# Performance work log

Hardware: AMD Instinct MI355X
Metric: run time of the kernel (lower is better)

## Reference

```python
import jax, jax.numpy as jnp
import numpy as np

L_DEG = 4      # max out-degree L
DEPTH = 7      # complete L-ary tree depth -> 21845 nodes
N_GEN = 16
C_ST = 8
M_LAB = 256


def _build_tree():
    sizes = [L_DEG ** d for d in range(DEPTH + 1)]
    limits = np.concatenate([[0], np.cumsum(sizes)]).astype(np.int64)
    t_size = int(limits[-1])
    nodes = np.arange(t_size)
    rng = np.random.default_rng(0)
    labels = rng.integers(0, M_LAB, t_size)
    parent = np.where(nodes > 0, (nodes - 1) // L_DEG, 0)
    pos = np.where(nodes > 0, (nodes - 1) % L_DEG, 0)
    ch = np.zeros((t_size, L_DEG), dtype=np.int64)
    n_internal = int(limits[-2])
    ch[:n_internal] = L_DEG * nodes[:n_internal, None] + np.arange(1, L_DEG + 1)[None, :]
    t = np.concatenate([labels[:, None], parent[:, None], pos[:, None], ch], axis=1).astype(np.int64)
    return t, limits


def setup_inputs() -> dict:
    key = jax.random.key(0)
    ka, kb, kp, ks = jax.random.split(key, 4)
    t, limits = _build_tree()
    return {
        "t": jnp.asarray(t),
        "t_limits": jnp.asarray(limits),
        "a": jax.random.normal(ka, (N_GEN, C_ST, C_ST, L_DEG), dtype=jnp.float32),
        "b": jax.random.normal(kb, (N_GEN, C_ST, M_LAB), dtype=jnp.float32),
        "pi": jax.random.normal(kp, (N_GEN, C_ST, L_DEG), dtype=jnp.float32),
        "sp": jax.random.normal(ks, (N_GEN, L_DEG), dtype=jnp.float32),
    }


def _forward(tn, lim, a, b, pi, sp):
    # tn, lim are host numpy int arrays (tree structure is a constant).
    G, C, _, L = a.shape
    t_size = int(lim[-1])
    n_levels = len(lim) - 1
    sL = int(lim[-2])                      # first leaf index
    labels = tn[:, 0]
    posf = tn[:, 2]
    ch_all = tn[:, 3:3 + L]

    sm_a = jax.nn.softmax(a, axis=1)       # P(parent_state i | child_state j, pos l)
    sm_b = jax.nn.softmax(b, axis=2)
    sm_pi = jax.nn.softmax(pi, axis=1)
    sm_sp = jax.nn.softmax(sp, axis=1)
    a_sp = sm_a * sm_sp[:, None, None, :]  # [G,i,j,L]

    # ---------------- upward pass ----------------
    prior = jnp.zeros((t_size, G, C), a.dtype)
    beta = jnp.zeros((t_size, G, C), a.dtype)
    beta_il = jnp.zeros((t_size, G, C), a.dtype)

    prior_lv = jnp.moveaxis(sm_pi[:, :, posf[sL:]], 2, 0)   # [NL,G,C]
    emis_lv = jnp.moveaxis(sm_b[:, :, labels[sL:]], 2, 0)   # [NL,G,C]
    beta_lv = prior_lv * emis_lv
    beta_lv = beta_lv / jnp.sum(beta_lv, axis=2, keepdims=True)
    prior = prior.at[sL:].set(prior_lv)
    beta = beta.at[sL:].set(beta_lv)

    for lev in range(n_levels - 2, -1, -1):   # internal levels, bottom-up
        s, e = int(lim[lev]), int(lim[lev + 1])
        ch = ch_all[s:e]                       # [P,L]
        mask = (ch > 0).astype(a.dtype)        # children packed in first slots
        prior_ch = prior[ch]                   # [P,L,G,C]
        beta_ch = beta[ch]                     # [P,L,G,C]
        u_prior = jnp.einsum('gijl,pl,plgj->pgi', a_sp, mask, prior_ch)
        u_bil = jnp.einsum('gijl,pl,plgj->pgi', a_sp, mask, beta_ch) / u_prior
        emis = jnp.moveaxis(sm_b[:, :, labels[s:e]], 2, 0)  # [P,G,C]
        tmp = emis * u_bil * u_prior
        u_beta = tmp / jnp.sum(tmp, axis=2, keepdims=True)
        prior = prior.at[s:e].set(u_prior)
        beta = beta.at[s:e].set(u_beta)
        beta_il = beta_il.at[s:e].set(u_bil)

    # ---------------- downward pass ----------------
    # row t_size is a dummy slot for padded (absent) children
    eps_i = jnp.zeros((t_size + 1, G, C), a.dtype).at[0].set(beta[0])
    eps_ijl = jnp.zeros((t_size, G, C, C, L), a.dtype)
    for lev in range(0, n_levels - 1):         # parents, top-down (root included)
        s, e = int(lim[lev]), int(lim[lev + 1])
        ch = ch_all[s:e]
        maskb = ch > 0
        mask = maskb.astype(a.dtype)
        beta_ch = jnp.transpose(beta[ch], (0, 2, 3, 1))       # [P,G,Cj,L]
        pe = eps_i[s:e] / (prior[s:e] * beta_il[s:e])         # [P,G,Ci]
        res = (pe[:, :, :, None, None] * a_sp[None]
               * beta_ch[:, :, None, :, :]
               * mask[:, None, None, None, :])                # [P,G,i,j,L]
        child_eps = jnp.sum(res, axis=3)                       # sum over j (as in source) -> [P,G,i,L]
        vals = jnp.moveaxis(child_eps, 3, 1).reshape(-1, G, C) # [P*L,G,C]
        safe = np.where(maskb, ch, t_size).reshape(-1)
        eps_i = eps_i.at[safe].set(vals)
        eps_ijl = eps_ijl.at[s:e].set(res)
    eps_i = eps_i[:t_size]
    # leaves' eps_ijl stay zero (source scatters zeros there)

    # ---------------- log-likelihood ----------------
    a_lh = jnp.einsum('ugijl,gijl->g', eps_ijl, jnp.log(sm_a))
    b_lh = jnp.einsum('ugc,gcu->g', eps_i, jnp.log(sm_b)[:, :, labels])
    pi_lh = jnp.einsum('ugc,gcu->g', eps_i[sL:], jnp.log(sm_pi)[:, :, posf[sL:]])
    eps_l = jnp.sum(eps_ijl, axis=(2, 3))                      # [u,g,L]
    sp_lh = jnp.einsum('ugl,gl->g', eps_l, jnp.log(sm_sp))
    return a_lh + b_lh + pi_lh + sp_lh


def reference(t, t_limits, a, b, pi, sp):
    tn = np.asarray(t)
    lim = np.asarray(t_limits)
    return _forward(tn, lim, a, b, pi, sp)
```

## Files before the change

### kernel.cpp

```cpp
#include <hip/hip_runtime.h>


#define G 16
#define C 8
#define GC 128
#define TSIZE 21845
#define SL 5461

__device__ __forceinline__ float grp8_sum(float v) {
  v += __shfl_xor(v, 1);
  v += __shfl_xor(v, 2);
  v += __shfl_xor(v, 4);
  return v;
}

__global__ void setup_kernel(const float* __restrict__ ain, const float* __restrict__ bin,
                             const float* __restrict__ piin, const float* __restrict__ spin,
                             float* __restrict__ a_sp, float* __restrict__ log_a,
                             float* __restrict__ sm_bT, float* __restrict__ log_bT,
                             float* __restrict__ sm_piT, float* __restrict__ log_piT,
                             float* __restrict__ log_sp, unsigned* __restrict__ ctr) {
  int blk = blockIdx.x, tid = threadIdx.x;
  if (blk < 16) {
    int g = blk;
    __shared__ float red4[4];
    for (int c = 0; c < 8; ++c) {
      int row = g * 8 + c;
      float x = bin[row * 256 + tid];
      float m = x;
      #pragma unroll
      for (int off2 = 32; off2; off2 >>= 1) m = fmaxf(m, __shfl_xor(m, off2));
      if ((tid & 63) == 0) red4[tid >> 6] = m;
      __syncthreads();
      m = fmaxf(fmaxf(red4[0], red4[1]), fmaxf(red4[2], red4[3]));
      __syncthreads();
      float e = expf(x - m);
      float ssum = e;
      #pragma unroll
      for (int off2 = 32; off2; off2 >>= 1) ssum += __shfl_xor(ssum, off2);
      if ((tid & 63) == 0) red4[tid >> 6] = ssum;
      __syncthreads();
      ssum = red4[0] + red4[1] + red4[2] + red4[3];
      __syncthreads();
      sm_bT[tid * GC + row]  = e / ssum;
      log_bT[tid * GC + row] = (x - m) - logf(ssum);
    }
  } else if (blk == 16) {
    for (int col = tid; col < 512; col += 256) {
      int g = col >> 5, j = (col >> 2) & 7, l = col & 3;
      float x[8], m = -1e30f;
      #pragma unroll
      for (int i = 0; i < 8; ++i) { x[i] = ain[g*256 + i*32 + j*4 + l]; m = fmaxf(m, x[i]); }
      float ssum = 0.f;
      #pragma unroll
      for (int i = 0; i < 8; ++i) ssum += expf(x[i] - m);
      float ls = logf(ssum);
      float y0 = spin[g*4+0], y1 = spin[g*4+1], y2 = spin[g*4+2], y3 = spin[g*4+3];
      float ms = fmaxf(fmaxf(y0, y1), fmaxf(y2, y3));
      float d = expf(y0-ms) + expf(y1-ms) + expf(y2-ms) + expf(y3-ms);
      float spv = expf(spin[g*4+l] - ms) / d;
      #pragma unroll
      for (int i = 0; i < 8; ++i) {
        int o2 = g*256 + i*32 + j*4 + l;
        float smv = expf(x[i] - m) / ssum;
        a_sp[o2]  = smv * spv;
        log_a[o2] = (x[i] - m) - ls;
      }
    }
  } else {
    if (tid < 64) {
      int g = tid >> 2, l = tid & 3;
      float x[8], m = -1e30f;
      #pragma unroll
      for (int c = 0; c < 8; ++c) { x[c] = piin[g*32 + c*4 + l]; m = fmaxf(m, x[c]); }
      float ssum = 0.f;
      #pragma unroll
      for (int c = 0; c < 8; ++c) ssum += expf(x[c] - m);
      float ls = logf(ssum);
      #pragma unroll
      for (int c = 0; c < 8; ++c) {
        sm_piT[l*GC + g*8 + c]  = expf(x[c] - m) / ssum;
        log_piT[l*GC + g*8 + c] = (x[c] - m) - ls;
      }
    } else if (tid < 80) {
      int g = tid - 64;
      float y[4], m = -1e30f;
      #pragma unroll
      for (int l = 0; l < 4; ++l) { y[l] = spin[g*4 + l]; m = fmaxf(m, y[l]); }
      float ssum = 0.f;
      #pragma unroll
      for (int l = 0; l < 4; ++l) ssum += expf(y[l] - m);
      float ls = logf(ssum);
      #pragma unroll
      for (int l = 0; l < 4; ++l) log_sp[g*4 + l] = (y[l] - m) - ls;
    } else if (tid == 80) {
      *ctr = 0u;
    }
  }
}

__device__ __forceinline__ void up_lds(int v, int lab, int gi, int g8,
    const float* asp, const float* __restrict__ sm_bT,
    float* sBeta, float* sNum, bool wantNum) {
  int ch0 = 4*v + 1;
  float ub = 0.f;
  #pragma unroll
  for (int l = 0; l < 4; ++l) {
    const float4* bp = (const float4*)(sBeta + (ch0 + l)*GC + g8);
    float4 b0 = bp[0], b1 = bp[1];
    ub += asp[l]*b0.x + asp[4+l]*b0.y + asp[8+l]*b0.z + asp[12+l]*b0.w
        + asp[16+l]*b1.x + asp[20+l]*b1.y + asp[24+l]*b1.z + asp[28+l]*b1.w;
  }
  float tmp = sm_bT[lab*GC + gi] * ub;
  float s = grp8_sum(tmp);
  sBeta[v*GC + gi] = tmp / s;
  if (wantNum) sNum[v*GC + gi] = ub;
}

__device__ __forceinline__ double down_lds(int v, int lab, float e, int gi, int g8,
    const float* asp, const float* aal, const float* lsp,
    const float* __restrict__ log_bT, float* sBeta, const float* sNum) {
  float pe = e / sNum[v*GC + gi];
  int ch0 = 4*v + 1;
  float local = 0.f;
  #pragma unroll
  for (int l = 0; l < 4; ++l) {
    float4* bp = (float4*)(sBeta + (ch0 + l)*GC + g8);
    float4 b0 = bp[0], b1 = bp[1];
    float S = asp[l]*b0.x + asp[4+l]*b0.y + asp[8+l]*b0.z + asp[12+l]*b0.w
            + asp[16+l]*b1.x + asp[20+l]*b1.y + asp[24+l]*b1.z + asp[28+l]*b1.w;
    float A = aal[l]*b0.x + aal[4+l]*b0.y + aal[8+l]*b0.z + aal[12+l]*b0.w
            + aal[16+l]*b1.x + aal[20+l]*b1.y + aal[24+l]*b1.z + aal[28+l]*b1.w;
    float ce = pe * S;
    sBeta[(ch0 + l)*GC + gi] = ce;
    local += pe*A + ce*lsp[l];
  }
  return (double)local + (double)(e * log_bT[lab*GC + gi]);
}

__global__ __launch_bounds__(512, 1) void up_kernel(
    const float* __restrict__ a_sp, const float* __restrict__ sm_bT,
    const float* __restrict__ sm_piT, const int* __restrict__ t,
    float* __restrict__ betaG) {
  __shared__ float sBeta[85*GC];
  const int blk = blockIdx.x, tid = threadIdx.x;
  const int gi = tid & 127, g = gi >> 3, i = gi & 7, g8 = g*8, w = tid >> 7;
  float asp[32];
  {
    const float4* pa = (const float4*)(a_sp + g*256 + i*32);
    #pragma unroll
    for (int q = 0; q < 8; ++q) {
      float4 v = pa[q];
      asp[q*4+0]=v.x; asp[q*4+1]=v.y; asp[q*4+2]=v.z; asp[q*4+3]=v.w;
    }
  }
  const int base_leaf = SL + blk*64;
  #pragma unroll
  for (int it = 0; it < 16; ++it) {
    int k = it*4 + w;
    float bt = sm_piT[(k & 3)*GC + gi] * sm_bT[t[(base_leaf + k)*7]*GC + gi];
    float s = grp8_sum(bt);
    sBeta[(21 + k)*GC + gi] = bt / s;
  }
  __syncthreads();
  #pragma unroll
  for (int it = 0; it < 4; ++it) {
    int k = it*4 + w;
    up_lds(5 + k, t[(1365 + blk*16 + k)*7], gi, g8, asp, sm_bT, sBeta, nullptr, false);
  }
  __syncthreads();
  up_lds(1 + w, t[(341 + blk*4 + w)*7], gi, g8, asp, sm_bT, sBeta, nullptr, false);
  __syncthreads();
  if (tid < 128) {
    up_lds(0, t[(85 + blk)*7], gi, g8, asp, sm_bT, sBeta, nullptr, false);
    betaG[(size_t)(85 + blk)*GC + gi] = sBeta[gi];
  }
}

__global__ __launch_bounds__(512, 1) void downall_kernel(
    const float* __restrict__ a_sp, const float* __restrict__ log_a,
    const float* __restrict__ log_sp, const float* __restrict__ sm_bT,
    const float* __restrict__ log_bT, const float* __restrict__ sm_piT,
    const float* __restrict__ log_piT, const int* __restrict__ t,
    const float* __restrict__ betaG, unsigned* __restrict__ ctr,
    double* __restrict__ partial, float* __restrict__ out) {
  __shared__ float  sBeta[85*GC];
  __shared__ float  sNum[21*GC];
  __shared__ float  sEps[GC];
  __shared__ double sd[64];
  __shared__ double sfin[256];
  __shared__ unsigned lastFlag;
  const int blk = blockIdx.x, tid = threadIdx.x;
  const int gi = tid & 127, g = gi >> 3, i = gi & 7, g8 = g*8, w = tid >> 7;
  float asp[32], aal[32], lsp[4];
  {
    const float4* pa = (const float4*)(a_sp  + g*256 + i*32);
    const float4* pl = (const float4*)(log_a + g*256 + i*32);
    #pragma unroll
    for (int k = 0; k < 8; ++k) {
      float4 va = pa[k], vl = pl[k];
      asp[k*4+0]=va.x; asp[k*4+1]=va.y; asp[k*4+2]=va.z; asp[k*4+3]=va.w;
      aal[k*4+0]=va.x*vl.x; aal[k*4+1]=va.y*vl.y; aal[k*4+2]=va.z*vl.z; aal[k*4+3]=va.w*vl.w;
    }
    #pragma unroll
    for (int l = 0; l < 4; ++l) lsp[l] = log_sp[g*4 + l];
  }

  #pragma unroll
  for (int it = 0; it < 16; ++it) {
    int k = it*4 + w, u = 21 + k;
    int ch0 = 4*u + 1;
    float ub = 0.f;
    #pragma unroll
    for (int l = 0; l < 4; ++l) {
      const float4* bp = (const float4*)(betaG + (size_t)(ch0 + l)*GC + g8);
      float4 b0 = bp[0], b1 = bp[1];
      ub += asp[l]*b0.x + asp[4+l]*b0.y + asp[8+l]*b0.z + asp[12+l]*b0.w
          + asp[16+l]*b1.x + asp[20+l]*b1.y + asp[24+l]*b1.z + asp[28+l]*b1.w;
    }
    float tmp = sm_bT[t[u*7]*GC + gi] * ub;
    float s = grp8_sum(tmp);
    sBeta[u*GC + gi] = tmp / s;
  }
  __syncthreads();
  #pragma unroll
  for (int it = 0; it < 4; ++it) {
    int u = 5 + it*4 + w;
    up_lds(u, t[u*7], gi, g8, asp, sm_bT, sBeta, sNum, true);
  }
  __syncthreads();
  up_lds(1 + w, t[(1 + w)*7], gi, g8, asp, sm_bT, sBeta, sNum, true);
  __syncthreads();
  if (tid < 128)
    up_lds(0, t[0], gi, g8, asp, sm_bT, sBeta, sNum, true);
  __syncthreads();

  double acc = 0.0;
  if (tid < 128) {
    int a1 = 1 + (blk >> 6), a2 = 5 + (blk >> 4), a3 = 21 + (blk >> 2);
    float e = sBeta[gi];
    int anc[3] = {0, a1, a2};
    int chn[3] = {a1, a2, a3};
    #pragma unroll
    for (int s2 = 0; s2 < 3; ++s2) {
      float pe = e / sNum[anc[s2]*GC + gi];
      int l = (chn[s2] - 1) & 3;
      const float4* bp = (const float4*)(sBeta + chn[s2]*GC + g8);
      float4 b0 = bp[0], b1 = bp[1];
      float S = asp[l]*b0.x + asp[4+l]*b0.y + asp[8+l]*b0.z + asp[12+l]*b0.w
              + asp[16+l]*b1.x + asp[20+l]*b1.y + asp[24+l]*b1.z + asp[28+l]*b1.w;
      e = pe * S;
    }
    float Sv[4], Av[4], num3 = 0.f;
    int c30 = 4*a3 + 1;
    #pragma unroll
    for (int l = 0; l < 4; ++l) {
      const float4* bp = (const float4*)(betaG + (size_t)(c30 + l)*GC + g8);
      float4 b0 = bp[0], b1 = bp[1];
      Sv[l] = asp[l]*b0.x + asp[4+l]*b0.y + asp[8+l]*b0.z + asp[12+l]*b0.w
            + asp[16+l]*b1.x + asp[20+l]*b1.y + asp[24+l]*b1.z + asp[28+l]*b1.w;
      num3 += Sv[l];
      Av[l] = aal[l]*b0.x + aal[4+l]*b0.y + aal[8+l]*b0.z + aal[12+l]*b0.w
            + aal[16+l]*b1.x + aal[20+l]*b1.y + aal[24+l]*b1.z + aal[28+l]*b1.w;
    }
    float e3 = e;
    float pe3 = e3 / num3;
    sEps[gi] = pe3 * Sv[blk & 3];
    if ((blk & 3) == 0) {
      float local = 0.f;
      #pragma unroll
      for (int l = 0; l < 4; ++l) local += pe3*Av[l] + (pe3*Sv[l])*lsp[l];
      acc += (double)local + (double)(e3 * log_bT[t[a3*7]*GC + gi]);
    }
  }
  __syncthreads();

  if (blk == 0) {
    if (tid < 128)
      acc += down_lds(0, t[0], sBeta[gi], gi, g8, asp, aal, lsp, log_bT, sBeta, sNum);
    __syncthreads();
    {
      int v = 1 + w;
      acc += down_lds(v, t[v*7], sBeta[v*GC + gi], gi, g8, asp, aal, lsp, log_bT, sBeta, sNum);
    }
    __syncthreads();
    #pragma unroll
    for (int it = 0; it < 4; ++it) {
      int v = 5 + it*4 + w;
      acc += down_lds(v, t[v*7], sBeta[v*GC + gi], gi, g8, asp, aal, lsp, log_bT, sBeta, sNum);
    }
    __syncthreads();
  }

  const int base_leaf = SL + blk*64;
  #pragma unroll
  for (int it = 0; it < 16; ++it) {
    int k = it*4 + w;
    float bt = sm_piT[(k & 3)*GC + gi] * sm_bT[t[(base_leaf + k)*7]*GC + gi];
    float s = grp8_sum(bt);
    sBeta[(21 + k)*GC + gi] = bt / s;
  }
  __syncthreads();
  #pragma unroll
  for (int it = 0; it < 4; ++it) {
    int k = it*4 + w;
    up_lds(5 + k, t[(1365 + blk*16 + k)*7], gi, g8, asp, sm_bT, sBeta, sNum, true);
  }
  __syncthreads();
  up_lds(1 + w, t[(341 + blk*4 + w)*7], gi, g8, asp, sm_bT, sBeta, sNum, true);
  __syncthreads();

  if (tid < 128) {
    up_lds(0, t[(85 + blk)*7], gi, g8, asp, sm_bT, sBeta, sNum, true);
    acc += down_lds(0, t[(85 + blk)*7], sEps[gi], gi, g8, asp, aal, lsp,
                    log_bT, sBeta, sNum);
  }
  __syncthreads();
  {
    int v = 1 + w;
    acc += down_lds(v, t[(341 + blk*4 + w)*7], sBeta[v*GC + gi], gi, g8,
                    asp, aal, lsp, log_bT, sBeta, sNum);
  }
  __syncthreads();
  #pragma unroll
  for (int it = 0; it < 4; ++it) {
    int k = it*4 + w, v = 5 + k;
    acc += down_lds(v, t[(1365 + blk*16 + k)*7], sBeta[v*GC + gi], gi, g8,
                    asp, aal, lsp, log_bT, sBeta, sNum);
  }
  __syncthreads();
  #pragma unroll
  for (int it = 0; it < 16; ++it) {
    int k = it*4 + w;
    float e = sBeta[(21 + k)*GC + gi];
    acc += (double)(e * (log_bT[t[(base_leaf + k)*7]*GC + gi] +
                         log_piT[(k & 3)*GC + gi]));
  }

  acc += __shfl_xor(acc, 1);
  acc += __shfl_xor(acc, 2);
  acc += __shfl_xor(acc, 4);
  if (i == 0) sd[tid >> 3] = acc;
  __syncthreads();
  if (tid < 16) partial[blk*16 + tid] = sd[tid] + sd[16 + tid] + sd[32 + tid] + sd[48 + tid];
  __syncthreads();

  if (tid == 0) {
    unsigned old = __hip_atomic_fetch_add(ctr, 1u, __ATOMIC_ACQ_REL,
                                          __HIP_MEMORY_SCOPE_AGENT);
    lastFlag = (old == 255u);
  }
  __syncthreads();
  if (lastFlag) {
    if (tid < 256) {
      int gg = tid & 15, ch = tid >> 4;
      const double* p = partial + (size_t)ch*256 + gg;
      double s = 0.0;
      #pragma unroll
      for (int q = 0; q < 16; ++q) s += p[q*16];
      sfin[tid] = s;
    }
    __syncthreads();
    if (tid < 16) {
      double tot = 0.0;
      #pragma unroll
      for (int ch = 0; ch < 16; ++ch) tot += sfin[ch*16 + tid];
      out[tid] = (float)tot;
    }
  }
}

extern "C" void kernel_launch(void* const* d_in, const int* in_sizes, int n_in,
                              void* d_out, int out_size, void* d_ws, size_t ws_size,
                              hipStream_t stream) {
  const int*   t  = (const int*)d_in[0];
  const float* a  = (const float*)d_in[2];
  const float* b  = (const float*)d_in[3];
  const float* pi = (const float*)d_in[4];
  const float* sp = (const float*)d_in[5];
  float* out = (float*)d_out;

  char* w = (char*)d_ws;
  size_t off = 0;
  auto carve = [&](size_t bytes) -> void* {
    void* ptr = w + off;
    off += (bytes + 255) & ~(size_t)255;
    return ptr;
  };
  float*    a_sp    = (float*)carve((size_t)16*8*8*4*4);
  float*    log_a   = (float*)carve((size_t)16*8*8*4*4);
  float*    sm_bT   = (float*)carve((size_t)256*GC*4);
  float*    log_bT  = (float*)carve((size_t)256*GC*4);
  float*    sm_piT  = (float*)carve((size_t)4*GC*4);
  float*    log_piT = (float*)carve((size_t)4*GC*4);
  float*    log_sp  = (float*)carve((size_t)16*4*4);
  float*    betaG   = (float*)carve((size_t)341*GC*4);
  double*   partial = (double*)carve((size_t)256*16*8);
  unsigned* ctr     = (unsigned*)carve((size_t)4);

  setup_kernel<<<18, 256, 0, stream>>>(a, b, pi, sp, a_sp, log_a, sm_bT, log_bT,
                                       sm_piT, log_piT, log_sp, ctr);
  up_kernel<<<256, 512, 0, stream>>>(a_sp, sm_bT, sm_piT, t, betaG);
  downall_kernel<<<256, 512, 0, stream>>>(a_sp, log_a, log_sp, sm_bT, log_bT,
                                          sm_piT, log_piT, t, betaG, ctr,
                                          partial, out);
}
```

Before: 111.0 us.

## Spill per-block upward subtree state to global and reload in down pass

```diff
diff --git a/kernel.cpp b/kernel.cpp
--- a/kernel.cpp
+++ b/kernel.cpp
@@ -21,31 +21,27 @@
                              float* __restrict__ sm_piT, float* __restrict__ log_piT,
                              float* __restrict__ log_sp, unsigned* __restrict__ ctr) {
   int blk = blockIdx.x, tid = threadIdx.x;
-  if (blk < 16) {
-    int g = blk;
+  if (blk < 128) {
     __shared__ float red4[4];
-    for (int c = 0; c < 8; ++c) {
-      int row = g * 8 + c;
-      float x = bin[row * 256 + tid];
-      float m = x;
-      #pragma unroll
-      for (int off2 = 32; off2; off2 >>= 1) m = fmaxf(m, __shfl_xor(m, off2));
-      if ((tid & 63) == 0) red4[tid >> 6] = m;
-      __syncthreads();
-      m = fmaxf(fmaxf(red4[0], red4[1]), fmaxf(red4[2], red4[3]));
-      __syncthreads();
-      float e = expf(x - m);
-      float ssum = e;
-      #pragma unroll
-      for (int off2 = 32; off2; off2 >>= 1) ssum += __shfl_xor(ssum, off2);
-      if ((tid & 63) == 0) red4[tid >> 6] = ssum;
-      __syncthreads();
-      ssum = red4[0] + red4[1] + red4[2] + red4[3];
-      __syncthreads();
-      sm_bT[tid * GC + row]  = e / ssum;
-      log_bT[tid * GC + row] = (x - m) - logf(ssum);
-    }
-  } else if (blk == 16) {
+    int row = blk;
+    float x = bin[row * 256 + tid];
+    float m = x;
+    #pragma unroll
+    for (int off2 = 32; off2; off2 >>= 1) m = fmaxf(m, __shfl_xor(m, off2));
+    if ((tid & 63) == 0) red4[tid >> 6] = m;
+    __syncthreads();
+    m = fmaxf(fmaxf(red4[0], red4[1]), fmaxf(red4[2], red4[3]));
+    __syncthreads();
+    float e = expf(x - m);
+    float ssum = e;
+    #pragma unroll
+    for (int off2 = 32; off2; off2 >>= 1) ssum += __shfl_xor(ssum, off2);
+    if ((tid & 63) == 0) red4[tid >> 6] = ssum;
+    __syncthreads();
+    ssum = red4[0] + red4[1] + red4[2] + red4[3];
+    sm_bT[tid * GC + row]  = e / ssum;
+    log_bT[tid * GC + row] = (x - m) - logf(ssum);
+  } else if (blk == 128) {
     for (int col = tid; col < 512; col += 256) {
       int g = col >> 5, j = (col >> 2) & 7, l = col & 3;
       float x[8], m = -1e30f;
@@ -141,8 +137,9 @@
 __global__ __launch_bounds__(512, 1) void up_kernel(
     const float* __restrict__ a_sp, const float* __restrict__ sm_bT,
     const float* __restrict__ sm_piT, const int* __restrict__ t,
-    float* __restrict__ betaG) {
+    float* __restrict__ betaS, float* __restrict__ numS) {
   __shared__ float sBeta[85*GC];
+  __shared__ float sNum[21*GC];
   const int blk = blockIdx.x, tid = threadIdx.x;
   const int gi = tid & 127, g = gi >> 3, i = gi & 7, g8 = g*8, w = tid >> 7;
   float asp[32];
@@ -166,14 +163,21 @@
   #pragma unroll
   for (int it = 0; it < 4; ++it) {
     int k = it*4 + w;
-    up_lds(5 + k, t[(1365 + blk*16 + k)*7], gi, g8, asp, sm_bT, sBeta, nullptr, false);
-  }
-  __syncthreads();
-  up_lds(1 + w, t[(341 + blk*4 + w)*7], gi, g8, asp, sm_bT, sBeta, nullptr, false);
-  __syncthreads();
-  if (tid < 128) {
-    up_lds(0, t[(85 + blk)*7], gi, g8, asp, sm_bT, sBeta, nullptr, false);
-    betaG[(size_t)(85 + blk)*GC + gi] = sBeta[gi];
+    up_lds(5 + k, t[(1365 + blk*16 + k)*7], gi, g8, asp, sm_bT, sBeta, sNum, true);
+  }
+  __syncthreads();
+  up_lds(1 + w, t[(341 + blk*4 + w)*7], gi, g8, asp, sm_bT, sBeta, sNum, true);
+  __syncthreads();
+  if (tid < 128)
+    up_lds(0, t[(85 + blk)*7], gi, g8, asp, sm_bT, sBeta, sNum, true);
+  __syncthreads();
+  {
+    const float4* srcB = (const float4*)sBeta;
+    float4* dstB = (float4*)(betaS + (size_t)blk*85*GC);
+    for (int n = tid; n < 85*GC/4; n += 512) dstB[n] = srcB[n];
+    const float4* srcN = (const float4*)sNum;
+    float4* dstN = (float4*)(numS + (size_t)blk*21*GC);
+    for (int n = tid; n < 21*GC/4; n += 512) dstN[n] = srcN[n];
   }
 }
 
@@ -182,8 +186,9 @@
     const float* __restrict__ log_sp, const float* __restrict__ sm_bT,
     const float* __restrict__ log_bT, const float* __restrict__ sm_piT,
     const float* __restrict__ log_piT, const int* __restrict__ t,
-    const float* __restrict__ betaG, unsigned* __restrict__ ctr,
-    double* __restrict__ partial, float* __restrict__ out) {
+    const float* __restrict__ betaS, const float* __restrict__ numS,
+    unsigned* __restrict__ ctr, double* __restrict__ partial,
+    float* __restrict__ out) {
   __shared__ float  sBeta[85*GC];
   __shared__ float  sNum[21*GC];
   __shared__ float  sEps[GC];
@@ -209,11 +214,10 @@
   #pragma unroll
   for (int it = 0; it < 16; ++it) {
     int k = it*4 + w, u = 21 + k;
-    int ch0 = 4*u + 1;
     float ub = 0.f;
     #pragma unroll
     for (int l = 0; l < 4; ++l) {
-      const float4* bp = (const float4*)(betaG + (size_t)(ch0 + l)*GC + g8);
+      const float4* bp = (const float4*)(betaS + (size_t)(4*k + l)*85*GC + g8);
       float4 b0 = bp[0], b1 = bp[1];
       ub += asp[l]*b0.x + asp[4+l]*b0.y + asp[8+l]*b0.z + asp[12+l]*b0.w
           + asp[16+l]*b1.x + asp[20+l]*b1.y + asp[24+l]*b1.z + asp[28+l]*b1.w;
@@ -252,10 +256,10 @@
       e = pe * S;
     }
     float Sv[4], Av[4], num3 = 0.f;
-    int c30 = 4*a3 + 1;
+    int qbase = blk & ~3;
     #pragma unroll
     for (int l = 0; l < 4; ++l) {
-      const float4* bp = (const float4*)(betaG + (size_t)(c30 + l)*GC + g8);
+      const float4* bp = (const float4*)(betaS + (size_t)(qbase + l)*85*GC + g8);
       float4 b0 = bp[0], b1 = bp[1];
       Sv[l] = asp[l]*b0.x + asp[4+l]*b0.y + asp[8+l]*b0.z + asp[12+l]*b0.w
             + asp[16+l]*b1.x + asp[20+l]*b1.y + asp[24+l]*b1.z + asp[28+l]*b1.w;
@@ -292,29 +296,20 @@
     __syncthreads();
   }
 
+  {
+    const float4* srcB = (const float4*)(betaS + (size_t)blk*85*GC);
+    float4* dstB = (float4*)sBeta;
+    for (int n = tid; n < 85*GC/4; n += 512) dstB[n] = srcB[n];
+    const float4* srcN = (const float4*)(numS + (size_t)blk*21*GC);
+    float4* dstN = (float4*)sNum;
+    for (int n = tid; n < 21*GC/4; n += 512) dstN[n] = srcN[n];
+  }
+  __syncthreads();
+
   const int base_leaf = SL + blk*64;
-  #pragma unroll
-  for (int it = 0; it < 16; ++it) {
-    int k = it*4 + w;
-    float bt = sm_piT[(k & 3)*GC + gi] * sm_bT[t[(base_leaf + k)*7]*GC + gi];
-    float s = grp8_sum(bt);
-    sBeta[(21 + k)*GC + gi] = bt / s;
-  }
-  __syncthreads();
-  #pragma unroll
-  for (int it = 0; it < 4; ++it) {
-    int k = it*4 + w;
-    up_lds(5 + k, t[(1365 + blk*16 + k)*7], gi, g8, asp, sm_bT, sBeta, sNum, true);
-  }
-  __syncthreads();
-  up_lds(1 + w, t[(341 + blk*4 + w)*7], gi, g8, asp, sm_bT, sBeta, sNum, true);
-  __syncthreads();
-
-  if (tid < 128) {
-    up_lds(0, t[(85 + blk)*7], gi, g8, asp, sm_bT, sBeta, sNum, true);
+  if (tid < 128)
     acc += down_lds(0, t[(85 + blk)*7], sEps[gi], gi, g8, asp, aal, lsp,
                     log_bT, sBeta, sNum);
-  }
   __syncthreads();
   {
     int v = 1 + w;
@@ -394,14 +389,15 @@
   float*    sm_piT  = (float*)carve((size_t)4*GC*4);
   float*    log_piT = (float*)carve((size_t)4*GC*4);
   float*    log_sp  = (float*)carve((size_t)16*4*4);
-  float*    betaG   = (float*)carve((size_t)341*GC*4);
+  float*    betaS   = (float*)carve((size_t)256*85*GC*4);
+  float*    numS    = (float*)carve((size_t)256*21*GC*4);
   double*   partial = (double*)carve((size_t)256*16*8);
   unsigned* ctr     = (unsigned*)carve((size_t)4);
 
-  setup_kernel<<<18, 256, 0, stream>>>(a, b, pi, sp, a_sp, log_a, sm_bT, log_bT,
-                                       sm_piT, log_piT, log_sp, ctr);
-  up_kernel<<<256, 512, 0, stream>>>(a_sp, sm_bT, sm_piT, t, betaG);
+  setup_kernel<<<130, 256, 0, stream>>>(a, b, pi, sp, a_sp, log_a, sm_bT, log_bT,
+                                        sm_piT, log_piT, log_sp, ctr);
+  up_kernel<<<256, 512, 0, stream>>>(a_sp, sm_bT, sm_piT, t, betaS, numS);
   downall_kernel<<<256, 512, 0, stream>>>(a_sp, log_a, log_sp, sm_bT, log_bT,
-                                          sm_piT, log_piT, t, betaG, ctr,
-                                          partial, out);
-}
+                                          sm_piT, log_piT, t, betaS, numS,
+                                          ctr, partial, out);
+}
```

Measured after the change: 107.1 us. 3.6% less time.
